# Kernel tuning notes

Measured on AMD Instinct MI355X. Metric: run time of the kernel, lower is better.

## Reference

```python
import jax, jax.numpy as jnp
import numpy as np
import math

B, S, D = 2048, 128, 64          # batch, seq_length, input_dim
H1, H2, OUT = 128, 128, 1        # sa_hidden, ta_hidden, output_dim


def _uniform(key, shape, stdv):
    return jax.random.uniform(key, shape, jnp.float32, -stdv, stdv)


def setup_inputs() -> dict:
    key = jax.random.key(0)
    ks = jax.random.split(key, 20)
    s1 = 1.0 / math.sqrt(H1)
    s2 = 1.0 / math.sqrt(H2)
    inp = {
        "X": jax.random.normal(ks[0], (B, S, D), jnp.float32),
        # SpatialLSTM params (stdv = 1/sqrt(sa_hidden))
        "sa_W": _uniform(ks[1], (D, 4 * H1), s1),
        "sa_U": _uniform(ks[2], (H1, 4 * H1), s1),
        "sa_b": _uniform(ks[3], (4 * H1,), s1),
        "sa_Wa": _uniform(ks[4], (D, D), s1),
        "sa_Ua": _uniform(ks[5], (2 * H1, D), s1),
        "sa_ba": _uniform(ks[6], (D,), s1),
        "sa_Va": _uniform(ks[7], (D, D), s1),
        # TemporalLSTM params (stdv = 1/sqrt(ta_hidden))
        "ta_Wa": _uniform(ks[8], (H1, S), s2),
        "ta_Ua": _uniform(ks[9], (H2, S), s2),
        "ta_ba": _uniform(ks[10], (S,), s2),
        "ta_Va": _uniform(ks[11], (S, S), s2),
        "ta_W": _uniform(ks[12], (H1, 4 * H2), s2),
        "ta_U": _uniform(ks[13], (H2, 4 * H2), s2),
        "ta_b": _uniform(ks[14], (4 * H2,), s2),
        "ta_Wy": _uniform(ks[15], (OUT, 4 * H2), s2),
        "fc_w": _uniform(ks[16], (OUT, H2), s2),
        "fc_b": _uniform(ks[17], (OUT,), s2),
    }
    return inp


def _sta_forward(X, sa_W, sa_U, sa_b, sa_Wa, sa_Ua, sa_ba, sa_Va,
                 ta_Wa, ta_Ua, ta_ba, ta_Va, ta_W, ta_U, ta_b, ta_Wy,
                 fc_w, fc_b):
    x = X[:, :, :D]                       # [B,S,D]
    y0 = X[:, 0, D - 1:].reshape(-1, OUT)  # y[:,0,:] -> [B,OUT]
    batch = x.shape[0]

    # ---- SpatialLSTM: scan over time ----
    def sa_step(carry, x_t):
        h, c = carry
        a = jnp.tanh(x_t @ sa_Wa + jnp.concatenate([h, c], axis=1) @ sa_Ua + sa_ba) @ sa_Va
        alpha = jax.nn.softmax(a, axis=1)            # [B,D]
        xw = alpha * x_t
        gates = xw @ sa_W + h @ sa_U + sa_b          # [B,4H1]
        i = jax.nn.sigmoid(gates[:, :H1])
        f = jax.nn.sigmoid(gates[:, H1:2 * H1])
        g = jnp.tanh(gates[:, 2 * H1:3 * H1])
        o = jax.nn.sigmoid(gates[:, 3 * H1:])
        c = f * c + i * g
        h = o * jnp.tanh(c)
        return (h, c), (h, alpha)

    h0 = jnp.zeros((batch, H1), X.dtype)
    c0 = jnp.zeros((batch, H1), X.dtype)
    _, (hs, alphas) = jax.lax.scan(sa_step, (h0, c0), jnp.swapaxes(x, 0, 1))
    H = jnp.swapaxes(hs, 0, 1)  # [B,S,H1]

    # ---- TemporalLSTM: scan over time, attending over the full H ----
    # note: s_t in the original stays zero for all t, so its s_t @ Ua term is 0.
    def ta_step(carry, h_t):
        lh, lc, y_prev = carry
        beta = jax.nn.softmax(jnp.tanh(h_t @ ta_Wa + ta_ba) @ ta_Va, axis=1)  # [B,S]
        h_att = jnp.einsum('bs,bsd->bd', beta, H)     # weighted sum over time
        gates = h_att @ ta_W + lh @ ta_U + y_prev @ ta_Wy + ta_b
        i = jax.nn.sigmoid(gates[:, :H2])
        f = jax.nn.sigmoid(gates[:, H2:2 * H2])
        g = jnp.tanh(gates[:, 2 * H2:3 * H2])
        o = jax.nn.sigmoid(gates[:, 3 * H2:])
        lc = f * lc + i * g
        lh = o * jnp.tanh(lc)
        y = lh @ fc_w.T + fc_b
        return (lh, lc, y), beta

    lh0 = jnp.zeros((batch, H2), X.dtype)
    lc0 = jnp.zeros((batch, H2), X.dtype)
    (_, _, y_pred), betas = jax.lax.scan(ta_step, (lh0, lc0, y0), jnp.swapaxes(H, 0, 1))
    return y_pred, alphas, betas  # alphas: [S,B,D], betas: [S,B,S]


def reference(X, sa_W, sa_U, sa_b, sa_Wa, sa_Ua, sa_ba, sa_Va,
              ta_Wa, ta_Ua, ta_ba, ta_Va, ta_W, ta_U, ta_b, ta_Wy,
              fc_w, fc_b):
    return _sta_forward(X, sa_W, sa_U, sa_b, sa_Wa, sa_Ua, sa_ba, sa_Va,
                        ta_Wa, ta_Ua, ta_ba, ta_Va, ta_W, ta_U, ta_b, ta_Wy,
                        fc_w, fc_b)
```

## Files before the change

### kernel.cpp

```cpp
#include <hip/hip_runtime.h>


#define BB 2048
#define SS 128
#define DD 64
#define HH 128
#define NG 512
#define M  8
#define NT 512

#define A_OFF    ((size_t)BB)
#define BETA_OFF ((size_t)BB + (size_t)SS*BB*DD)
#define H_BYTES  ((size_t)BB*SS*HH*4)
#define G0_BYTES ((size_t)BB*SS*NG*4)

#define B1G_ELEMS (192*512)
#define B1A_ELEMS (320*64)
#define BVA_ELEMS (64*64)
#define B3_ELEMS  (256*512)
#define BW_ELEMS  (128*128)
#define GH_OFF 0
#define GL_OFF (B1G_ELEMS)
#define AH_OFF (2*B1G_ELEMS)
#define AL_OFF (2*B1G_ELEMS + B1A_ELEMS)
// ... 45 lines not shown
{
  int id = blockIdx.x*256 + threadIdx.x;
  if (id < B1G_ELEMS){
    int k = id >> 9, n = id & 511;
    float v = (k < 128) ? saU[(size_t)k*NG + n] : saW[(size_t)(k-128)*NG + n];
    int kk = k >> 5, kw = k & 31, nt = n >> 4, nc = n & 15;
    int lane = ((kw >> 3) << 4) | nc, j = kw & 7;
    size_t off = ((size_t)(nt*6 + kk)*64 + lane)*8 + j;
    unsigned short hi = bf16rne(v);
    F[GH_OFF + off] = hi; F[GL_OFF + off] = bf16rne(v - bfval(hi));
  }
  if (id < B1A_ELEMS){
    int k = id >> 6, n = id & 63;
    float v = (k < 256) ? saUa[(size_t)k*DD + n] : saWa[(size_t)(k-256)*DD + n];
    int kt = k >> 5, kw = k & 31, nt = n >> 4, nc = n & 15;
    int lane = ((kw >> 3) << 4) | nc, j = kw & 7;
    size_t off = ((size_t)(nt*10 + kt)*64 + lane)*8 + j;
    unsigned short hi = bf16rne(v);
    F[AH_OFF + off] = hi; F[AL_OFF + off] = bf16rne(v - bfval(hi));
  }
  if (id < BVA_ELEMS){
    int k = id >> 6, n = id & 63;
    float v = saVa[(size_t)k*DD + n];
    int kt = k >> 5, kw = k & 31, nt = n >> 4, nc = n & 15;
    int lane = ((kw >> 3) << 4) | nc, j = kw & 7;
    size_t off = ((size_t)(nt*2 + kt)*64 + lane)*8 + j;
    unsigned short hi = bf16rne(v);
    F[VH_OFF + off] = hi; F[VL_OFF + off] = bf16rne(v - bfval(hi));
  }
  if (id < B3_ELEMS){
    int k = id >> 9, n = id & 511;
    float v = (k < HH) ? taU[(size_t)k*NG + n] : taW[(size_t)(k-HH)*NG + n];
    int kt = k >> 5, kw = k & 31, nt = n >> 4, nc = n & 15;
    int lane = ((kw >> 3) << 4) | nc, j = kw & 7;
    size_t off = ((size_t)(nt*8 + kt)*64 + lane)*8 + j;
    unsigned short hi = bf16rne(v);
    F[B3H_OFF + off] = hi; F[B3L_OFF + off] = bf16rne(v - bfval(hi));
  }
  if (id < BW_ELEMS){
    int k = id >> 7, n = id & 127;
    int kt = k >> 5, kw = k & 31, nt = n >> 4, nc = n & 15;
    int lane = ((kw >> 3) << 4) | nc, j = kw & 7;
    size_t off = ((size_t)(nt*4 + kt)*64 + lane)*8 + j;
    F[RW_OFF + off] = bf16rne(taWa[(size_t)k*SS + n]);
    F[RV_OFF + off] = bf16rne(taVa[(size_t)k*SS + n]);
  }
}

struct P1 {
  uint4 afh[12*64];
  uint4 afl[12*64];
  uint4 aah[2*64];
  uint4 aal[2*64];
  float xx[M][DD];
  float cc[M][HH];
  float red[2][M][64];
  float g[M][NG];
  float sbias[NG];
};
struct P2S { float A[32][HH]; float tmp[32][SS]; float bp[32][SS]; };
union __align__(16) SMA { P1 p1; float pad[21504]; };

__global__ __launch_bounds__(NT, 2) __attribute__((amdgpu_waves_per_eu(2, 2)))
void mf_ph1_kernel(
    const float* __restrict__ X,   const float* __restrict__ sab,
    const float* __restrict__ saba,
    const unsigned short* __restrict__ Fr,
    float* __restrict__ out, float* __restrict__ Hws)
{
  __shared__ SMA sm;
  const int tid = threadIdx.x;
  const int b0  = blockIdx.x * M;
  const int w   = tid >> 6, l = tid & 63;

  {
    uint4 z4 = make_uint4(0,0,0,0);
    for (int i = tid; i < 12*64; i += NT){ sm.p1.afh[i] = z4; sm.p1.afl[i] = z4; }
    if (tid < 2*64){ sm.p1.aah[tid] = z4; sm.p1.aal[tid] = z4; }
    for (int i = tid; i < M*HH; i += NT) ((float*)sm.p1.cc)[i] = 0.f;
    sm.p1.sbias[tid] = sab[tid];
  }
  __syncthreads();
  if (tid < 128){
    int r = tid >> 4, d0 = (tid & 15)*4;
    float4 v = *(const float4*)(X + (size_t)(b0+r)*SS*DD + d0);
    *(float4*)&sm.p1.xx[r][d0] = v;
    unsigned short* AFH = (unsigned short*)sm.p1.afh;
    unsigned short* AFL = (unsigned short*)sm.p1.afl;
    int kt = 8 + (d0 >> 5), lane = (((d0 & 31) >> 3) << 4) | r, jj0 = d0 & 7;
    float vv[4] = {v.x, v.y, v.z, v.w};
#pragma unroll
    for (int p = 0; p < 4; ++p){
      unsigned short h_ = bf16rne(vv[p]);
      AFH[(kt*64 + lane)*8 + jj0 + p] = h_;
      AFL[(kt*64 + lane)*8 + jj0 + p] = bf16rne(vv[p] - bfval(h_));
    }
  }
  __syncthreads();

  for (int t = 0; t < SS; ++t){
    f32x4 accg[4];
    {
      f32x4 zf = {0.f,0.f,0.f,0.f};
#pragma unroll
      for (int n4 = 0; n4 < 4; ++n4) accg[n4] = zf;
    }
    {
      const int nt = w & 3, kh = w >> 2;
      f32x4 a0 = {0.f,0.f,0.f,0.f}, a1 = {0.f,0.f,0.f,0.f};
      const uint4* BAH = (const uint4*)(Fr + AH_OFF);
      const uint4* BAL = (const uint4*)(Fr + AL_OFF);
#pragma unroll
      for (int q = 0; q < 5; ++q){
        const int kt = kh*5 + q;
        bf16x8 ah = as_bf(sm.p1.afh[kt*64 + l]);
        bf16x8 av = as_bf(sm.p1.afl[kt*64 + l]);
        bf16x8 bh = as_bf(BAH[(nt*10 + kt)*64 + l]);
        bf16x8 bl = as_bf(BAL[(nt*10 + kt)*64 + l]);
        if (q & 1){
          a1 = __builtin_amdgcn_mfma_f32_16x16x32_bf16(ah, bh, a1, 0, 0, 0);
          a1 = __builtin_amdgcn_mfma_f32_16x16x32_bf16(av, bh, a1, 0, 0, 0);
          a1 = __builtin_amdgcn_mfma_f32_16x16x32_bf16(ah, bl, a1, 0, 0, 0);
        } else {
          a0 = __builtin_amdgcn_mfma_f32_16x16x32_bf16(ah, bh, a0, 0, 0, 0);
          a0 = __builtin_amdgcn_mfma_f32_16x16x32_bf16(av, bh, a0, 0, 0, 0);
          a0 = __builtin_amdgcn_mfma_f32_16x16x32_bf16(ah, bl, a0, 0, 0, 0);
        }
      }
      f32x4 acc = a0 + a1;
      const int row0 = (l >> 4)*4, c0 = l & 15;
      if (row0 < 8){
#pragma unroll
        for (int jj = 0; jj < 4; ++jj)
          sm.p1.red[kh][row0+jj][nt*16 + c0] = acc[jj];
      }
      const uint4* GH = (const uint4*)(Fr + GH_OFF);
      const uint4* GL = (const uint4*)(Fr + GL_OFF);
#pragma unroll
      for (int kk = 0; kk < 4; ++kk){
        bf16x8 ah = as_bf(sm.p1.afh[kk*64 + l]);
        bf16x8 av = as_bf(sm.p1.afl[kk*64 + l]);
#pragma unroll
        for (int n4 = 0; n4 < 4; ++n4){
          const int ntg = w*4 + n4;
          bf16x8 bh = as_bf(GH[(ntg*6 + kk)*64 + l]);
          bf16x8 bl = as_bf(GL[(ntg*6 + kk)*64 + l]);
          accg[n4] = __builtin_amdgcn_mfma_f32_16x16x32_bf16(ah, bh, accg[n4], 0, 0, 0);
          accg[n4] = __builtin_amdgcn_mfma_f32_16x16x32_bf16(av, bh, accg[n4], 0, 0, 0);
          accg[n4] = __builtin_amdgcn_mfma_f32_16x16x32_bf16(ah, bl, accg[n4], 0, 0, 0);
        }
      }
    }
    __syncthreads();

    {
      const int r = w, col = l;
      float s = sm.p1.red[0][r][col] + sm.p1.red[1][r][col] + saba[col];
      float av = tanhx(s);
      unsigned short h_ = bf16rne(av);
      int kt = col >> 5, lane = (((col & 31) >> 3) << 4) | r, jj = col & 7;
      ((unsigned short*)sm.p1.aah)[(kt*64 + lane)*8 + jj] = h_;
      ((unsigned short*)sm.p1.aal)[(kt*64 + lane)*8 + jj] = bf16rne(av - bfval(h_));
    }
    __syncthreads();

    {
      const int nt = w & 3, kt = w >> 2;
      f32x4 acc = {0.f,0.f,0.f,0.f};
      bf16x8 ah = as_bf(sm.p1.aah[kt*64 + l]);
      bf16x8 av = as_bf(sm.p1.aal[kt*64 + l]);
      bf16x8 bh = as_bf(((const uint4*)(Fr + VH_OFF))[(nt*2 + kt)*64 + l]);
      bf16x8 bl = as_bf(((const uint4*)(Fr + VL_OFF))[(nt*2 + kt)*64 + l]);
      acc = __builtin_amdgcn_mfma_f32_16x16x32_bf16(ah, bh, acc, 0, 0, 0);
      acc = __builtin_amdgcn_mfma_f32_16x16x32_bf16(av, bh, acc, 0, 0, 0);
      acc = __builtin_amdgcn_mfma_f32_16x16x32_bf16(ah, bl, acc, 0, 0, 0);
      const int row0 = (l >> 4)*4, c0 = l & 15;
      if (row0 < 8){
#pragma unroll
        for (int jj = 0; jj < 4; ++jj)
          sm.p1.red[kt][row0+jj][nt*16 + c0] = acc[jj];
      }
    }
    __syncthreads();

    {
      const int r = w, col = l;
      float s = sm.p1.red[0][r][col] + sm.p1.red[1][r][col];
      float mm = wmax64(s);
      float e  = __expf(s - mm);
      float alv = e * (1.0f / wsum64(e));
      out[A_OFF + (size_t)t*BB*DD + (size_t)(b0+r)*DD + col] = alv;
      float xwv = alv * sm.p1.xx[r][col];
      unsigned short h_ = bf16rne(xwv);
      int kt = 10 + (col >> 5), lane = (((col & 31) >> 3) << 4) | r, jj = col & 7;
      ((unsigned short*)sm.p1.afh)[(kt*64 + lane)*8 + jj] = h_;
      ((unsigned short*)sm.p1.afl)[(kt*64 + lane)*8 + jj] = bf16rne(xwv - bfval(h_));
    }
    __syncthreads();

    float4 pf;
    const bool dox = (tid < 128) && (t + 1 < SS);
    if (dox){
      int r = tid >> 4, d0 = (tid & 15)*4;
      pf = *(const float4*)(X + (size_t)(b0+r)*SS*DD + (size_t)(t+1)*DD + d0);
    }
    {
      const uint4* GH = (const uint4*)(Fr + GH_OFF);
      const uint4* GL = (const uint4*)(Fr + GL_OFF);
#pragma unroll
      for (int kk = 4; kk < 6; ++kk){
        const int afi = kk + 6;
        bf16x8 ah = as_bf(sm.p1.afh[afi*64 + l]);
        bf16x8 av = as_bf(sm.p1.afl[afi*64 + l]);
#pragma unroll
        for (int n4 = 0; n4 < 4; ++n4){
          const int ntg = w*4 + n4;
          bf16x8 bh = as_bf(GH[(ntg*6 + kk)*64 + l]);
          bf16x8 bl = as_bf(GL[(ntg*6 + kk)*64 + l]);
          accg[n4] = __builtin_amdgcn_mfma_f32_16x16x32_bf16(ah, bh, accg[n4], 0, 0, 0);
          accg[n4] = __builtin_amdgcn_mfma_f32_16x16x32_bf16(av, bh, accg[n4], 0, 0, 0);
          accg[n4] = __builtin_amdgcn_mfma_f32_16x16x32_bf16(ah, bl, accg[n4], 0, 0, 0);
        }
      }
      const int row0 = (l >> 4)*4, c0 = l & 15;
      if (row0 < 8){
#pragma unroll
        for (int n4 = 0; n4 < 4; ++n4){
          int col = w*64 + n4*16 + c0;
          float b = sm.p1.sbias[col];
#pragma unroll
          for (int jj = 0; jj < 4; ++jj)
            sm.p1.g[row0+jj][col] = accg[n4][jj] + b;
        }
      }
    }
    __syncthreads();

    {
      unsigned short* AFH = (unsigned short*)sm.p1.afh;
      unsigned short* AFL = (unsigned short*)sm.p1.afl;
#pragma unroll
      for (int h2 = 0; h2 < 2; ++h2){
        int idx = h2*NT + tid;
        int r = idx >> 7, j = idx & 127;
        float iv = sigf (sm.p1.g[r][j]);
        float fv = sigf (sm.p1.g[r][j + 128]);
        float gv = tanhx(sm.p1.g[r][j + 256]);
        float ov = sigf (sm.p1.g[r][j + 384]);
        float cn = fv * sm.p1.cc[r][j] + iv * gv;
        float hn = ov * tanhx(cn);
        sm.p1.cc[r][j] = cn;
        Hws[(size_t)(b0+r)*SS*HH + (size_t)t*HH + j] = hn;
        int lane = (((j & 31) >> 3) << 4) | r, jj = j & 7;
        int ktH = j >> 5, ktC = 4 + (j >> 5);
        unsigned short hh_ = bf16rne(hn);
        unsigned short ch_ = bf16rne(cn);
        AFH[(ktH*64 + lane)*8 + jj] = hh_;
        AFL[(ktH*64 + lane)*8 + jj] = bf16rne(hn - bfval(hh_));
        AFH[(ktC*64 + lane)*8 + jj] = ch_;
        AFL[(ktC*64 + lane)*8 + jj] = bf16rne(cn - bfval(ch_));
      }
      if (dox){
        int r = tid >> 4, d0 = (tid & 15)*4;
        *(float4*)&sm.p1.xx[r][d0] = pf;
        int kt = 8 + (d0 >> 5), lane = (((d0 & 31) >> 3) << 4) | r, jj0 = d0 & 7;
        float vv[4] = {pf.x, pf.y, pf.z, pf.w};
#pragma unroll
        for (int p = 0; p < 4; ++p){
          unsigned short h_ = bf16rne(vv[p]);
          AFH[(kt*64 + lane)*8 + jj0 + p] = h_;
          AFL[(kt*64 + lane)*8 + jj0 + p] = bf16rne(vv[p] - bfval(h_));
        }
      }
    }
    __syncthreads();
  }
}

struct PH2SM {
  union {
    struct { uint4 fA[8][4][64]; uint4 fB[8][4][64]; } f;
    float HO[128][132];
  } u;
  unsigned short S[128][136];
  float bias[SS];
};

__global__ __launch_bounds__(NT, 2) void ph2_kernel(
    const float* __restrict__ taba, const unsigned short* __restrict__ Fr,
    float* __restrict__ out, float* __restrict__ Hws)
{
  __shared__ PH2SM sm;
  const int tid = threadIdx.x;
  const int b   = blockIdx.x;
  const int w   = tid >> 6, l = tid & 63;
  const int g   = l >> 4, c0 = l & 15;
  float* Hb = Hws + (size_t)b * SS * HH;

  if (tid < SS) sm.bias[tid] = taba[tid];
  {
    const float4* src = (const float4*)Hb;
#pragma unroll
    for (int i = 0; i < 8; ++i){
      int fidx = i*NT + tid;
      float4 v = src[fidx];
      int e0 = fidx*4, row = e0 >> 7, col = e0 & 127;
      sm.S[row][col+0] = bf16rne(v.x);
      sm.S[row][col+1] = bf16rne(v.y);
      sm.S[row][col+2] = bf16rne(v.z);
      sm.S[row][col+3] = bf16rne(v.w);
    }
  }
  __syncthreads();

#pragma unroll
  for (int i = 0; i < 4; ++i){
    int slot = i*NT + tid;
    int mt = slot >> 8, kt = (slot >> 6) & 3, ll = slot & 63;
    int row = mt*16 + (ll & 15), k0 = kt*32 + (ll >> 4)*8;
    ((uint4*)sm.u.f.fA)[slot] = *(const uint4*)&sm.S[row][k0];
  }
#pragma unroll
  for (int i = 0; i < 4; ++i){
    int slot = i*NT + tid;
    int nt = slot >> 8, kt = (slot >> 6) & 3, ll = slot & 63;
    int col = nt*16 + (ll & 15), s0 = kt*32 + (ll >> 4)*8;
// ... 63 lines not shown
    for (int nt = 1; nt < 8; ++nt) m = fmaxf(m, acc[nt][j]);
#pragma unroll
    for (int ms = 1; ms < 16; ms <<= 1) m = fmaxf(m, __shfl_xor(m, ms, 64));
    float e[8], s = 0.f;
#pragma unroll
    for (int nt = 0; nt < 8; ++nt){ e[nt] = __expf(acc[nt][j] - m); s += e[nt]; }
#pragma unroll
    for (int ms = 1; ms < 16; ms <<= 1) s += __shfl_xor(s, ms, 64);
    float inv = 1.0f / s;
    int row = w*16 + g*4 + j;
    size_t bo = BETA_OFF + (size_t)row*BB*SS + (size_t)b*SS;
#pragma unroll
    for (int nt = 0; nt < 8; ++nt){
      float bv = e[nt] * inv;
      out[bo + nt*16 + c0] = bv;
      sm.S[row][nt*16 + c0] = bf16rne(bv);
    }
  }
  __syncthreads();

#pragma unroll
  for (int i = 0; i < 4; ++i){
    int slot = i*NT + tid;
    int mt = slot >> 8, kt = (slot >> 6) & 3, ll = slot & 63;
    int row = mt*16 + (ll & 15), k0 = kt*32 + (ll >> 4)*8;
    ((uint4*)sm.u.f.fA)[slot] = *(const uint4*)&sm.S[row][k0];
  }
  __syncthreads();

#pragma unroll
  for (int nt = 0; nt < 8; ++nt) acc[nt] = zero4;
#pragma unroll
  for (int kt = 0; kt < 4; ++kt){
    bf16x8 a = as_bf(sm.u.f.fA[w][kt][l]);
#pragma unroll
    for (int nt = 0; nt < 8; ++nt){
      bf16x8 bv = as_bf(sm.u.f.fB[nt][kt][l]);
      acc[nt] = __builtin_amdgcn_mfma_f32_16x16x32_bf16(a, bv, acc[nt], 0, 0, 0);
    }
  }
  __syncthreads();

#pragma unroll
  for (int nt = 0; nt < 8; ++nt)
#pragma unroll
    for (int j = 0; j < 4; ++j)
      sm.u.HO[w*16 + g*4 + j][nt*16 + c0] = acc[nt][j];
  __syncthreads();
#pragma unroll
  for (int it = 0; it < 8; ++it){
    int flat = it*NT + tid;
    int row = flat >> 5, cq = flat & 31;
    *(float4*)(Hb + (size_t)row*HH + cq*4) = *(const float4*)&sm.u.HO[row][cq*4];
  }
}

struct GMM { uint4 afh[8][4][64]; uint4 afl[8][4][64]; float SG[128][132]; };

__global__ __launch_bounds__(NT, 2) void g0mm_kernel(
    const float* __restrict__ Ha, const unsigned short* __restrict__ Fr,
    const float* __restrict__ tab, float* __restrict__ G0)
{
  __shared__ GMM sm;
  const int tid = threadIdx.x;
  const size_t r0 = (size_t)blockIdx.x * 128;
  const int w = tid >> 6, l = tid & 63;
  const int row0 = (l >> 4)*4, c0 = l & 15;

  {
    const float4* src = (const float4*)(Ha + r0*HH);
    unsigned short* AFH = (unsigned short*)sm.afh;
    unsigned short* AFL = (unsigned short*)sm.afl;
#pragma unroll
    for (int i = 0; i < 8; ++i){
      int f = i*NT + tid;
      float4 v = src[f];
      int e0 = f*4, rl = e0 >> 7, k0 = e0 & 127;
      int mt = rl >> 4, kt = k0 >> 5;
      int lane = (((k0 & 31) >> 3) << 4) | (rl & 15), j0 = k0 & 7;
      size_t base = ((size_t)(mt*4 + kt)*64 + lane)*8 + j0;
      float vv[4] = {v.x, v.y, v.z, v.w};
#pragma unroll
      for (int p = 0; p < 4; ++p){
        unsigned short h_ = bf16rne(vv[p]);
        AFH[base + p] = h_;
        AFL[base + p] = bf16rne(vv[p] - bfval(h_));
      }
    }
  }
  __syncthreads();

  const uint4* BH = (const uint4*)(Fr + B3H_OFF);
  const uint4* BL = (const uint4*)(Fr + B3L_OFF);
#pragma unroll
  for (int p = 0; p < 4; ++p){
    const int nt = p*8 + w;
    uint4 bh[4], bl[4];
#pragma unroll
    for (int kt = 0; kt < 4; ++kt){
      bh[kt] = BH[(nt*8 + 4 + kt)*64 + l];
      bl[kt] = BL[(nt*8 + 4 + kt)*64 + l];
    }
    const float tb = tab[nt*16 + c0];
    f32x4 zero4 = {0.f,0.f,0.f,0.f};
    f32x4 acc[8];
#pragma unroll
    for (int mt = 0; mt < 8; ++mt) acc[mt] = zero4;
#pragma unroll
    for (int mt = 0; mt < 8; ++mt){
#pragma unroll
      for (int kt = 0; kt < 4; ++kt){
        bf16x8 ah = as_bf(sm.afh[mt][kt][l]);
        bf16x8 av = as_bf(sm.afl[mt][kt][l]);
        bf16x8 vbh = as_bf(bh[kt]);
        bf16x8 vbl = as_bf(bl[kt]);
        acc[mt] = __builtin_amdgcn_mfma_f32_16x16x32_bf16(ah, vbh, acc[mt], 0, 0, 0);
        acc[mt] = __builtin_amdgcn_mfma_f32_16x16x32_bf16(av, vbh, acc[mt], 0, 0, 0);
        acc[mt] = __builtin_amdgcn_mfma_f32_16x16x32_bf16(ah, vbl, acc[mt], 0, 0, 0);
      }
    }
#pragma unroll
    for (int mt = 0; mt < 8; ++mt)
#pragma unroll
      for (int j = 0; j < 4; ++j)
        sm.SG[mt*16 + row0 + j][w*16 + c0] = acc[mt][j] + tb;
    __syncthreads();
#pragma unroll
    for (int it = 0; it < 8; ++it){
      int flat = it*NT + tid;
      int row = flat >> 5, cq = flat & 31;
      *(float4*)(G0 + (r0 + row)*NG + p*128 + cq*4) = *(const float4*)&sm.SG[row][cq*4];
    }
    __syncthreads();
  }
}

struct P3H {
  uint4 afh[4*64];
  uint4 afl[4*64];
  float lh[M][HH];
  float lc[M][HH];
  float g[M][NG];
  float wy[NG];
  float fcv[HH];
  float yp[M];
};
union __align__(16) SMCH { P3H s; float pad[21504]; };

__global__ __launch_bounds__(NT, 2) __attribute__((amdgpu_waves_per_eu(2, 2)))
void mf_ph3h_kernel(
    const float* __restrict__ X, const unsigned short* __restrict__ Fr,
    const float* __restrict__ G0,
    const float* __restrict__ taWy,
    const float* __restrict__ fcw, const float* __restrict__ fcb,
    float* __restrict__ out)
{
  __shared__ SMCH sm;
  const int tid = threadIdx.x;
  const int b0  = blockIdx.x * M;
  const int w   = tid >> 6, l = tid & 63;
  const int row0 = (l >> 4)*4, c0 = l & 15;

  {
    uint4 z4 = make_uint4(0,0,0,0);
    if (tid < 4*64){ sm.s.afh[tid] = z4; sm.s.afl[tid] = z4; }
    for (int i = tid; i < M*HH; i += NT){
      ((float*)sm.s.lh)[i] = 0.f; ((float*)sm.s.lc)[i] = 0.f;
    }
    sm.s.wy[tid] = taWy[tid];
    if (tid < HH) sm.s.fcv[tid] = fcw[tid];
    if (tid < M)  sm.s.yp[tid] = X[(size_t)(b0+tid)*SS*DD + (DD-1)];
  }
  __syncthreads();

  for (int t = 0; t < SS; ++t){
    {
      float g0v[16];
      if (row0 < 8){
#pragma unroll
        for (int n4 = 0; n4 < 4; ++n4){
#pragma unroll
          for (int j = 0; j < 4; ++j)
            g0v[n4*4+j] = G0[((size_t)(b0+row0+j)*SS + t)*NG + (w*64 + n4*16 + c0)];
        }
      }
      f32x4 zero4 = {0.f,0.f,0.f,0.f};
      f32x4 acc[4];
#pragma unroll
      for (int n4 = 0; n4 < 4; ++n4) acc[n4] = zero4;
      const uint4* BH = (const uint4*)(Fr + B3H_OFF);
      const uint4* BL = (const uint4*)(Fr + B3L_OFF);
#pragma unroll
      for (int kt = 0; kt < 4; ++kt){
        bf16x8 ah = as_bf(sm.s.afh[kt*64 + l]);
        bf16x8 av = as_bf(sm.s.afl[kt*64 + l]);
#pragma unroll
        for (int n4 = 0; n4 < 4; ++n4){
          const int ntg = w*4 + n4;
          bf16x8 bh = as_bf(BH[(ntg*8 + kt)*64 + l]);
          bf16x8 bl = as_bf(BL[(ntg*8 + kt)*64 + l]);
          acc[n4] = __builtin_amdgcn_mfma_f32_16x16x32_bf16(ah, bh, acc[n4], 0, 0, 0);
          acc[n4] = __builtin_amdgcn_mfma_f32_16x16x32_bf16(av, bh, acc[n4], 0, 0, 0);
          acc[n4] = __builtin_amdgcn_mfma_f32_16x16x32_bf16(ah, bl, acc[n4], 0, 0, 0);
        }
      }
      if (row0 < 8){
#pragma unroll
        for (int n4 = 0; n4 < 4; ++n4){
          int col = w*64 + n4*16 + c0;
          float wv = sm.s.wy[col];
#pragma unroll
          for (int j = 0; j < 4; ++j)
            sm.s.g[row0+j][col] = acc[n4][j] + g0v[n4*4+j] + sm.s.yp[row0+j]*wv;
        }
      }
    }
    __syncthreads();

    {
      unsigned short* AFH = (unsigned short*)sm.s.afh;
      unsigned short* AFL = (unsigned short*)sm.s.afl;
#pragma unroll
      for (int h2 = 0; h2 < 2; ++h2){
        int idx = h2*NT + tid;
        int r = idx >> 7, j = idx & 127;
        float iv = sigf (sm.s.g[r][j]);
        float fv = sigf (sm.s.g[r][j + 128]);
        float gv = tanhx(sm.s.g[r][j + 256]);
        float ov = sigf (sm.s.g[r][j + 384]);
        float cn = fv * sm.s.lc[r][j] + iv * gv;
        float hn = ov * tanhx(cn);
        sm.s.lc[r][j] = cn; sm.s.lh[r][j] = hn;
        int kt = j >> 5, lane = (((j & 31) >> 3) << 4) | r, jj = j & 7;
        unsigned short h_ = bf16rne(hn);
        AFH[(kt*64 + lane)*8 + jj] = h_;
        AFL[(kt*64 + lane)*8 + jj] = bf16rne(hn - bfval(h_));
      }
    }
    __syncthreads();

    {
      const int r = w, lx = l;
      float p = sm.s.lh[r][lx]*sm.s.fcv[lx] + sm.s.lh[r][lx+64]*sm.s.fcv[lx+64];
      p = wsum64(p);
      if (lx == 0) sm.s.yp[r] = p + fcb[0];
    }
    __syncthreads();
  }

  if (tid < M) out[b0 + tid] = sm.s.yp[tid];
}

struct P3 {
  uint4 afh[8*64];
  uint4 afl[8*64];
  float lh[M][HH];
  float lc[M][HH];
  float g[M][NG];
  float sb[NG];
  float wy[NG];
  float fcv[HH];
  float yp[M];
};
union __align__(16) SMC { P3 s; float pad[21504]; };

__global__ __launch_bounds__(NT, 2) void mf_ph3_kernel(
    const float* __restrict__ X, const float* __restrict__ Ha,
    const unsigned short* __restrict__ Fr,
    const float* __restrict__ tab, const float* __restrict__ taWy,
    const float* __restrict__ fcw, const float* __restrict__ fcb,
    float* __restrict__ out)
{
  __shared__ SMC sm;
  const int tid = threadIdx.x;
  const int b0  = blockIdx.x * M;
  const int w   = tid >> 6, l = tid & 63;

  {
    uint4 z4 = make_uint4(0,0,0,0);
    sm.s.afh[tid] = z4; sm.s.afl[tid] = z4;
    for (int i = tid; i < M*HH; i += NT){
      ((float*)sm.s.lh)[i] = 0.f; ((float*)sm.s.lc)[i] = 0.f;
    }
    sm.s.sb[tid] = tab[tid];
    sm.s.wy[tid] = taWy[tid];
    if (tid < HH) sm.s.fcv[tid] = fcw[tid];
    if (tid < M)  sm.s.yp[tid] = X[(size_t)(b0+tid)*SS*DD + (DD-1)];
  }
  __syncthreads();
  if (tid < 256){
    int r = tid >> 5, d0 = (tid & 31)*4;
    float4 v = *(const float4*)(Ha + (size_t)(b0+r)*SS*HH + d0);
    unsigned short* AFH = (unsigned short*)sm.s.afh;
    unsigned short* AFL = (unsigned short*)sm.s.afl;
    int kt = 4 + (d0 >> 5), lane = (((d0 & 31) >> 3) << 4) | r, jj0 = d0 & 7;
    float vv[4] = {v.x, v.y, v.z, v.w};
#pragma unroll
    for (int p = 0; p < 4; ++p){
// ... 399 lines not shown
      float gv = tanhx(s.g[r][j + 2*HH]);
      float ov = sigf (s.g[r][j + 3*HH]);
      float cn = fv * s.lc[r][j] + iv * gv;
      float hn = ov * tanhx(cn);
      s.lc[r][j] = cn; s.lh[r][j] = hn;
    }
    if (t + 1 < SS && tid < M*HH/4){
      int r = tid >> 5, q = tid & 31;
      ((float4*)s.ha)[tid] =
        *(const float4*)(Ha + (size_t)(b0+r)*SS*HH + (size_t)(t+1)*HH + q*4);
    }
    __syncthreads();
    {
      const int r = tid >> 6, lx = tid & 63;
      float p = s.lh[r][lx]*fcw[lx] + s.lh[r][lx+64]*fcw[lx+64];
      p = wsum64(p);
      if (lx == 0) s.yp[r] = p + fcb[0];
    }
    __syncthreads();
  }
  if (tid < M) out[b0 + tid] = s.yp[tid];
}

extern "C" void kernel_launch(void* const* d_in, const int* in_sizes, int n_in,
                              void* d_out, int out_size, void* d_ws, size_t ws_size,
                              hipStream_t stream) {
  (void)in_sizes; (void)n_in; (void)out_size;
  const float* X    = (const float*)d_in[0];
  const float* saW  = (const float*)d_in[1];
  const float* saU  = (const float*)d_in[2];
  const float* sab  = (const float*)d_in[3];
  const float* saWa = (const float*)d_in[4];
  const float* saUa = (const float*)d_in[5];
  const float* saba = (const float*)d_in[6];
  const float* saVa = (const float*)d_in[7];
  const float* taWa = (const float*)d_in[8];
  const float* taba = (const float*)d_in[10];
  const float* taVa = (const float*)d_in[11];
  const float* taW  = (const float*)d_in[12];
  const float* taU  = (const float*)d_in[13];
  const float* tab  = (const float*)d_in[14];
  const float* taWy = (const float*)d_in[15];
  const float* fcw  = (const float*)d_in[16];
  const float* fcb  = (const float*)d_in[17];
  float* out = (float*)d_out;

  if (ws_size >= NEED2_BYTES){
    unsigned short* Fr = (unsigned short*)d_ws;
    float* Hws = (float*)((char*)d_ws + FRAG_BYTES);
    hipLaunchKernelGGL(repack_kernel, dim3(512), dim3(256), 0, stream,
                       saW, saU, saWa, saUa, saVa, taU, taW, taWa, taVa, Fr);
    hipLaunchKernelGGL(mf_ph1_kernel, dim3(BB / M), dim3(NT), 0, stream,
                       X, sab, saba, Fr, out, Hws);
    hipLaunchKernelGGL(ph2_kernel, dim3(BB), dim3(NT), 0, stream,
                       taba, Fr, out, Hws);
    if (ws_size >= NEED3_BYTES){
      float* G0 = (float*)((char*)d_ws + FRAG_BYTES + H_BYTES);
      hipLaunchKernelGGL(g0mm_kernel, dim3((BB*SS)/128), dim3(NT), 0, stream,
                         Hws, Fr, tab, G0);
      hipLaunchKernelGGL(mf_ph3h_kernel, dim3(BB / M), dim3(NT), 0, stream,
                         X, Fr, G0, taWy, fcw, fcb, out);
    } else {
      hipLaunchKernelGGL(mf_ph3_kernel, dim3(BB / M), dim3(NT), 0, stream,
                         X, Hws, Fr, tab, taWy, fcw, fcb, out);
    }
  } else {
    float* Hws = (float*)d_ws;
    hipLaunchKernelGGL(fb_ph12_kernel, dim3(BB / M), dim3(NT), 0, stream,
                       X, saW, saU, sab, saWa, saUa, saba, saVa,
                       taWa, taba, taVa, out, Hws);
    hipLaunchKernelGGL(fb_ph3_kernel, dim3(BB / M), dim3(NT), 0, stream,
                       X, Hws, taW, taU, tab, taWy, fcw, fcb, out);
  }
}
```

Before: 1.621 ms.

## Fuse temporal attention with G0 projection, cache spatial weights in LDS, prefetch G0

Adds a ph2g kernel that computes the temporal attention (beta and h_att) per batch element and immediately multiplies h_att by the input weights to write the precomputed gate term G0. This replaces the separate ph2 and g0mm kernels and avoids writing h_att to global memory and reading it back. The spatial-phase kernel now stages the attention weight fragments (Ua/Wa and Va) in shared memory once instead of re-reading them from global memory every timestep. The temporal recurrent kernel prefetches the next step's G0 values into registers. The extra LDS in the spatial kernel may reduce occupancy.

Measured after the change: 1.432 ms. 1.13x faster.

```diff
diff --git a/kernel.cpp b/kernel.cpp
--- a/kernel.cpp
+++ b/kernel.cpp
@@ -121,6 +121,10 @@
   uint4 afl[12*64];
   uint4 aah[2*64];
   uint4 aal[2*64];
+  uint4 awh[2560];
+  uint4 awl[2560];
+  uint4 vh[512];
+  uint4 vl[512];
   float xx[M][DD];
   float cc[M][HH];
   float red[2][M][64];
@@ -128,7 +132,6 @@
   float sbias[NG];
 };
 struct P2S { float A[32][HH]; float tmp[32][SS]; float bp[32][SS]; };
-union __align__(16) SMA { P1 p1; float pad[21504]; };
 
 __global__ __launch_bounds__(NT, 2) __attribute__((amdgpu_waves_per_eu(2, 2)))
 void mf_ph1_kernel(
@@ -137,25 +140,30 @@
     const unsigned short* __restrict__ Fr,
     float* __restrict__ out, float* __restrict__ Hws)
 {
-  __shared__ SMA sm;
+  __shared__ P1 sm;
   const int tid = threadIdx.x;
   const int b0  = blockIdx.x * M;
   const int w   = tid >> 6, l = tid & 63;
 
   {
     uint4 z4 = make_uint4(0,0,0,0);
-    for (int i = tid; i < 12*64; i += NT){ sm.p1.afh[i] = z4; sm.p1.afl[i] = z4; }
-    if (tid < 2*64){ sm.p1.aah[tid] = z4; sm.p1.aal[tid] = z4; }
-    for (int i = tid; i < M*HH; i += NT) ((float*)sm.p1.cc)[i] = 0.f;
-    sm.p1.sbias[tid] = sab[tid];
+    for (int i = tid; i < 12*64; i += NT){ sm.afh[i] = z4; sm.afl[i] = z4; }
+    if (tid < 2*64){ sm.aah[tid] = z4; sm.aal[tid] = z4; }
+    for (int i = tid; i < M*HH; i += NT) ((float*)sm.cc)[i] = 0.f;
+    sm.sbias[tid] = sab[tid];
+    const uint4* sh = (const uint4*)(Fr + AH_OFF);
+    const uint4* sl = (const uint4*)(Fr + AL_OFF);
+    for (int i = tid; i < 2560; i += NT){ sm.awh[i] = sh[i]; sm.awl[i] = sl[i]; }
+    sm.vh[tid] = ((const uint4*)(Fr + VH_OFF))[tid];
+    sm.vl[tid] = ((const uint4*)(Fr + VL_OFF))[tid];
   }
   __syncthreads();
   if (tid < 128){
     int r = tid >> 4, d0 = (tid & 15)*4;
     float4 v = *(const float4*)(X + (size_t)(b0+r)*SS*DD + d0);
-    *(float4*)&sm.p1.xx[r][d0] = v;
-    unsigned short* AFH = (unsigned short*)sm.p1.afh;
-    unsigned short* AFL = (unsigned short*)sm.p1.afl;
+    *(float4*)&sm.xx[r][d0] = v;
+    unsigned short* AFH = (unsigned short*)sm.afh;
+    unsigned short* AFL = (unsigned short*)sm.afl;
     int kt = 8 + (d0 >> 5), lane = (((d0 & 31) >> 3) << 4) | r, jj0 = d0 & 7;
     float vv[4] = {v.x, v.y, v.z, v.w};
 #pragma unroll
@@ -177,15 +185,13 @@
     {
       const int nt = w & 3, kh = w >> 2;
       f32x4 a0 = {0.f,0.f,0.f,0.f}, a1 = {0.f,0.f,0.f,0.f};
-      const uint4* BAH = (const uint4*)(Fr + AH_OFF);
-      const uint4* BAL = (const uint4*)(Fr + AL_OFF);
 #pragma unroll
       for (int q = 0; q < 5; ++q){
         const int kt = kh*5 + q;
-        bf16x8 ah = as_bf(sm.p1.afh[kt*64 + l]);
-        bf16x8 av = as_bf(sm.p1.afl[kt*64 + l]);
-        bf16x8 bh = as_bf(BAH[(nt*10 + kt)*64 + l]);
-        bf16x8 bl = as_bf(BAL[(nt*10 + kt)*64 + l]);
+        bf16x8 ah = as_bf(sm.afh[kt*64 + l]);
+        bf16x8 av = as_bf(sm.afl[kt*64 + l]);
+        bf16x8 bh = as_bf(sm.awh[(nt*10 + kt)*64 + l]);
+        bf16x8 bl = as_bf(sm.awl[(nt*10 + kt)*64 + l]);
         if (q & 1){
           a1 = __builtin_amdgcn_mfma_f32_16x16x32_bf16(ah, bh, a1, 0, 0, 0);
           a1 = __builtin_amdgcn_mfma_f32_16x16x32_bf16(av, bh, a1, 0, 0, 0);
@@ -201,14 +207,14 @@
       if (row0 < 8){
 #pragma unroll
         for (int jj = 0; jj < 4; ++jj)
-          sm.p1.red[kh][row0+jj][nt*16 + c0] = acc[jj];
+          sm.red[kh][row0+jj][nt*16 + c0] = acc[jj];
       }
       const uint4* GH = (const uint4*)(Fr + GH_OFF);
       const uint4* GL = (const uint4*)(Fr + GL_OFF);
 #pragma unroll
       for (int kk = 0; kk < 4; ++kk){
-        bf16x8 ah = as_bf(sm.p1.afh[kk*64 + l]);
-        bf16x8 av = as_bf(sm.p1.afl[kk*64 + l]);
+        bf16x8 ah = as_bf(sm.afh[kk*64 + l]);
+        bf16x8 av = as_bf(sm.afl[kk*64 + l]);
 #pragma unroll
         for (int n4 = 0; n4 < 4; ++n4){
           const int ntg = w*4 + n4;
@@ -224,22 +230,22 @@
 
     {
       const int r = w, col = l;
-      float s = sm.p1.red[0][r][col] + sm.p1.red[1][r][col] + saba[col];
+      float s = sm.red[0][r][col] + sm.red[1][r][col] + saba[col];
       float av = tanhx(s);
       unsigned short h_ = bf16rne(av);
       int kt = col >> 5, lane = (((col & 31) >> 3) << 4) | r, jj = col & 7;
-      ((unsigned short*)sm.p1.aah)[(kt*64 + lane)*8 + jj] = h_;
-      ((unsigned short*)sm.p1.aal)[(kt*64 + lane)*8 + jj] = bf16rne(av - bfval(h_));
+      ((unsigned short*)sm.aah)[(kt*64 + lane)*8 + jj] = h_;
+      ((unsigned short*)sm.aal)[(kt*64 + lane)*8 + jj] = bf16rne(av - bfval(h_));
     }
     __syncthreads();
 
     {
       const int nt = w & 3, kt = w >> 2;
       f32x4 acc = {0.f,0.f,0.f,0.f};
-      bf16x8 ah = as_bf(sm.p1.aah[kt*64 + l]);
-      bf16x8 av = as_bf(sm.p1.aal[kt*64 + l]);
-      bf16x8 bh = as_bf(((const uint4*)(Fr + VH_OFF))[(nt*2 + kt)*64 + l]);
-      bf16x8 bl = as_bf(((const uint4*)(Fr + VL_OFF))[(nt*2 + kt)*64 + l]);
+      bf16x8 ah = as_bf(sm.aah[kt*64 + l]);
+      bf16x8 av = as_bf(sm.aal[kt*64 + l]);
+      bf16x8 bh = as_bf(sm.vh[(nt*2 + kt)*64 + l]);
+      bf16x8 bl = as_bf(sm.vl[(nt*2 + kt)*64 + l]);
       acc = __builtin_amdgcn_mfma_f32_16x16x32_bf16(ah, bh, acc, 0, 0, 0);
       acc = __builtin_amdgcn_mfma_f32_16x16x32_bf16(av, bh, acc, 0, 0, 0);
       acc = __builtin_amdgcn_mfma_f32_16x16x32_bf16(ah, bl, acc, 0, 0, 0);
@@ -247,23 +253,23 @@
       if (row0 < 8){
 #pragma unroll
         for (int jj = 0; jj < 4; ++jj)
-          sm.p1.red[kt][row0+jj][nt*16 + c0] = acc[jj];
+          sm.red[kt][row0+jj][nt*16 + c0] = acc[jj];
       }
     }
     __syncthreads();
 
     {
       const int r = w, col = l;
-      float s = sm.p1.red[0][r][col] + sm.p1.red[1][r][col];
+      float s = sm.red[0][r][col] + sm.red[1][r][col];
       float mm = wmax64(s);
       float e  = __expf(s - mm);
       float alv = e * (1.0f / wsum64(e));
       out[A_OFF + (size_t)t*BB*DD + (size_t)(b0+r)*DD + col] = alv;
-      float xwv = alv * sm.p1.xx[r][col];
+      float xwv = alv * sm.xx[r][col];
       unsigned short h_ = bf16rne(xwv);
       int kt = 10 + (col >> 5), lane = (((col & 31) >> 3) << 4) | r, jj = col & 7;
-      ((unsigned short*)sm.p1.afh)[(kt*64 + lane)*8 + jj] = h_;
-      ((unsigned short*)sm.p1.afl)[(kt*64 + lane)*8 + jj] = bf16rne(xwv - bfval(h_));
+      ((unsigned short*)sm.afh)[(kt*64 + lane)*8 + jj] = h_;
+      ((unsigned short*)sm.afl)[(kt*64 + lane)*8 + jj] = bf16rne(xwv - bfval(h_));
     }
     __syncthreads();
 
@@ -279,8 +285,8 @@
 #pragma unroll
       for (int kk = 4; kk < 6; ++kk){
         const int afi = kk + 6;
-        bf16x8 ah = as_bf(sm.p1.afh[afi*64 + l]);
-        bf16x8 av = as_bf(sm.p1.afl[afi*64 + l]);
+        bf16x8 ah = as_bf(sm.afh[afi*64 + l]);
+        bf16x8 av = as_bf(sm.afl[afi*64 + l]);
 #pragma unroll
         for (int n4 = 0; n4 < 4; ++n4){
           const int ntg = w*4 + n4;
@@ -296,29 +302,29 @@
 #pragma unroll
         for (int n4 = 0; n4 < 4; ++n4){
           int col = w*64 + n4*16 + c0;
-          float b = sm.p1.sbias[col];
+          float b = sm.sbias[col];
 #pragma unroll
           for (int jj = 0; jj < 4; ++jj)
-            sm.p1.g[row0+jj][col] = accg[n4][jj] + b;
-        }
-      }
-    }
-    __syncthreads();
-
-    {
-      unsigned short* AFH = (unsigned short*)sm.p1.afh;
-      unsigned short* AFL = (unsigned short*)sm.p1.afl;
+            sm.g[row0+jj][col] = accg[n4][jj] + b;
+        }
+      }
+    }
+    __syncthreads();
+
+    {
+      unsigned short* AFH = (unsigned short*)sm.afh;
+      unsigned short* AFL = (unsigned short*)sm.afl;
 #pragma unroll
       for (int h2 = 0; h2 < 2; ++h2){
         int idx = h2*NT + tid;
         int r = idx >> 7, j = idx & 127;
-        float iv = sigf (sm.p1.g[r][j]);
-        float fv = sigf (sm.p1.g[r][j + 128]);
-        float gv = tanhx(sm.p1.g[r][j + 256]);
-        float ov = sigf (sm.p1.g[r][j + 384]);
-        float cn = fv * sm.p1.cc[r][j] + iv * gv;
+        float iv = sigf (sm.g[r][j]);
+        float fv = sigf (sm.g[r][j + 128]);
+        float gv = tanhx(sm.g[r][j + 256]);
+        float ov = sigf (sm.g[r][j + 384]);
+        float cn = fv * sm.cc[r][j] + iv * gv;
         float hn = ov * tanhx(cn);
-        sm.p1.cc[r][j] = cn;
+        sm.cc[r][j] = cn;
         Hws[(size_t)(b0+r)*SS*HH + (size_t)t*HH + j] = hn;
         int lane = (((j & 31) >> 3) << 4) | r, jj = j & 7;
         int ktH = j >> 5, ktC = 4 + (j >> 5);
@@ -331,7 +337,7 @@
       }
       if (dox){
         int r = tid >> 4, d0 = (tid & 15)*4;
-        *(float4*)&sm.p1.xx[r][d0] = pf;
+        *(float4*)&sm.xx[r][d0] = pf;
         int kt = 8 + (d0 >> 5), lane = (((d0 & 31) >> 3) << 4) | r, jj0 = d0 & 7;
         float vv[4] = {pf.x, pf.y, pf.z, pf.w};
 #pragma unroll
@@ -341,6 +347,220 @@
           AFL[(kt*64 + lane)*8 + jj0 + p] = bf16rne(vv[p] - bfval(h_));
         }
       }
+    }
+    __syncthreads();
+  }
+}
+
+struct PH2G {
+  union { unsigned short S[128][136]; float SG[128][68]; } u1;
+  unsigned short S2[128][136];
+  uint4 fA[8][4][64];
+  uint4 fB[8][4][64];
+  float bias[SS];
+};
+
+__global__ __launch_bounds__(NT, 2) void ph2g_kernel(
+    const float* __restrict__ taba, const unsigned short* __restrict__ Fr,
+    const float* __restrict__ tab,
+    float* __restrict__ out, float* __restrict__ Hws, float* __restrict__ G0)
+{
+  __shared__ PH2G sm;
+  const int tid = threadIdx.x;
+  const int b   = blockIdx.x;
+  const int w   = tid >> 6, l = tid & 63;
+  const int g   = l >> 4, c0 = l & 15;
+  const float* Hb = Hws + (size_t)b * SS * HH;
+
+  if (tid < SS) sm.bias[tid] = taba[tid];
+  {
+    const float4* src = (const float4*)Hb;
+#pragma unroll
+    for (int i = 0; i < 8; ++i){
+      int fidx = i*NT + tid;
+      float4 v = src[fidx];
+      int e0 = fidx*4, row = e0 >> 7, col = e0 & 127;
+      sm.u1.S[row][col+0] = bf16rne(v.x);
+      sm.u1.S[row][col+1] = bf16rne(v.y);
+      sm.u1.S[row][col+2] = bf16rne(v.z);
+      sm.u1.S[row][col+3] = bf16rne(v.w);
+    }
+  }
+  __syncthreads();
+
+#pragma unroll
+  for (int i = 0; i < 4; ++i){
+    int slot = i*NT + tid;
+    int mt = slot >> 8, kt = (slot >> 6) & 3, ll = slot & 63;
+    int row = mt*16 + (ll & 15), k0 = kt*32 + (ll >> 4)*8;
+    ((uint4*)sm.fA)[slot] = *(const uint4*)&sm.u1.S[row][k0];
+  }
+#pragma unroll
+  for (int i = 0; i < 4; ++i){
+    int slot = i*NT + tid;
+    int nt = slot >> 8, kt = (slot >> 6) & 3, ll = slot & 63;
+    int col = nt*16 + (ll & 15), s0 = kt*32 + (ll >> 4)*8;
+    unsigned u[4];
+#pragma unroll
+    for (int p = 0; p < 4; ++p)
+      u[p] = (unsigned)sm.u1.S[s0+2*p][col] | ((unsigned)sm.u1.S[s0+2*p+1][col] << 16);
+    ((uint4*)sm.fB)[slot] = make_uint4(u[0], u[1], u[2], u[3]);
+  }
+  __syncthreads();
+
+  f32x4 acc[8];
+  f32x4 zero4 = {0.f, 0.f, 0.f, 0.f};
+
+#pragma unroll
+  for (int nt = 0; nt < 8; ++nt) acc[nt] = zero4;
+  {
+    const uint4* BW = (const uint4*)(Fr + RW_OFF);
+#pragma unroll
+    for (int kt = 0; kt < 4; ++kt){
+      bf16x8 a = as_bf(sm.fA[w][kt][l]);
+#pragma unroll
+      for (int nt = 0; nt < 8; ++nt){
+        bf16x8 bv = as_bf(BW[(nt*4 + kt)*64 + l]);
+        acc[nt] = __builtin_amdgcn_mfma_f32_16x16x32_bf16(a, bv, acc[nt], 0, 0, 0);
+      }
+    }
+  }
+#pragma unroll
+  for (int nt = 0; nt < 8; ++nt){
+    int col = nt*16 + c0;
+    float bv = sm.bias[col];
+#pragma unroll
+    for (int j = 0; j < 4; ++j)
+      sm.u1.S[w*16 + g*4 + j][col] = bf16rne(tanhx(acc[nt][j] + bv));
+  }
+  __syncthreads();
+
+#pragma unroll
+  for (int i = 0; i < 4; ++i){
+    int slot = i*NT + tid;
+    int mt = slot >> 8, kt = (slot >> 6) & 3, ll = slot & 63;
+    int row = mt*16 + (ll & 15), k0 = kt*32 + (ll >> 4)*8;
+    ((uint4*)sm.fA)[slot] = *(const uint4*)&sm.u1.S[row][k0];
+  }
+  __syncthreads();
+
+#pragma unroll
+  for (int nt = 0; nt < 8; ++nt) acc[nt] = zero4;
+  {
+    const uint4* BV = (const uint4*)(Fr + RV_OFF);
+#pragma unroll
+    for (int kt = 0; kt < 4; ++kt){
+      bf16x8 a = as_bf(sm.fA[w][kt][l]);
+#pragma unroll
+      for (int nt = 0; nt < 8; ++nt){
+        bf16x8 bv = as_bf(BV[(nt*4 + kt)*64 + l]);
+        acc[nt] = __builtin_amdgcn_mfma_f32_16x16x32_bf16(a, bv, acc[nt], 0, 0, 0);
+      }
+    }
+  }
+
+#pragma unroll
+  for (int j = 0; j < 4; ++j){
+    float m = acc[0][j];
+#pragma unroll
+    for (int nt = 1; nt < 8; ++nt) m = fmaxf(m, acc[nt][j]);
+#pragma unroll
+    for (int ms = 1; ms < 16; ms <<= 1) m = fmaxf(m, __shfl_xor(m, ms, 64));
+    float e[8], s = 0.f;
+#pragma unroll
+    for (int nt = 0; nt < 8; ++nt){ e[nt] = __expf(acc[nt][j] - m); s += e[nt]; }
+#pragma unroll
+    for (int ms = 1; ms < 16; ms <<= 1) s += __shfl_xor(s, ms, 64);
+    float inv = 1.0f / s;
+    int row = w*16 + g*4 + j;
+    size_t bo = BETA_OFF + (size_t)row*BB*SS + (size_t)b*SS;
+#pragma unroll
+    for (int nt = 0; nt < 8; ++nt){
+      float bv = e[nt] * inv;
+      out[bo + nt*16 + c0] = bv;
+      sm.u1.S[row][nt*16 + c0] = bf16rne(bv);
+    }
+  }
+  __syncthreads();
+
+#pragma unroll
+  for (int i = 0; i < 4; ++i){
+    int slot = i*NT + tid;
+    int mt = slot >> 8, kt = (slot >> 6) & 3, ll = slot & 63;
+    int row = mt*16 + (ll & 15), k0 = kt*32 + (ll >> 4)*8;
+    ((uint4*)sm.fA)[slot] = *(const uint4*)&sm.u1.S[row][k0];
+  }
+  __syncthreads();
+
+#pragma unroll
+  for (int nt = 0; nt < 8; ++nt) acc[nt] = zero4;
+#pragma unroll
+  for (int kt = 0; kt < 4; ++kt){
+    bf16x8 a = as_bf(sm.fA[w][kt][l]);
+#pragma unroll
+    for (int nt = 0; nt < 8; ++nt){
+      bf16x8 bv = as_bf(sm.fB[nt][kt][l]);
+      acc[nt] = __builtin_amdgcn_mfma_f32_16x16x32_bf16(a, bv, acc[nt], 0, 0, 0);
+    }
+  }
+#pragma unroll
+  for (int nt = 0; nt < 8; ++nt){
+#pragma unroll
+    for (int j = 0; j < 4; ++j){
+      int row = w*16 + g*4 + j, col = nt*16 + c0;
+      float v = acc[nt][j];
+      unsigned short h_ = bf16rne(v);
+      sm.u1.S[row][col] = h_;
+      sm.S2[row][col]   = bf16rne(v - bfval(h_));
+    }
+  }
+  __syncthreads();
+
+#pragma unroll
+  for (int i = 0; i < 4; ++i){
+    int slot = i*NT + tid;
+    int mt = slot >> 8, kt = (slot >> 6) & 3, ll = slot & 63;
+    int row = mt*16 + (ll & 15), k0 = kt*32 + (ll >> 4)*8;
+    ((uint4*)sm.fA)[slot] = *(const uint4*)&sm.u1.S[row][k0];
+    ((uint4*)sm.fB)[slot] = *(const uint4*)&sm.S2[row][k0];
+  }
+  __syncthreads();
+
+  const uint4* BH = (const uint4*)(Fr + B3H_OFF);
+  const uint4* BL = (const uint4*)(Fr + B3L_OFF);
+  const size_t r0 = (size_t)b * SS;
+#pragma unroll
+  for (int p = 0; p < 8; ++p){
+    f32x4 acc2[4];
+#pragma unroll
+    for (int q = 0; q < 4; ++q) acc2[q] = zero4;
+#pragma unroll
+    for (int q = 0; q < 4; ++q){
+      const int ntg = p*4 + q;
+#pragma unroll
+      for (int kt = 0; kt < 4; ++kt){
+        bf16x8 ah = as_bf(sm.fA[w][kt][l]);
+        bf16x8 av = as_bf(sm.fB[w][kt][l]);
+        bf16x8 bh = as_bf(BH[(ntg*8 + 4 + kt)*64 + l]);
+        bf16x8 bl = as_bf(BL[(ntg*8 + 4 + kt)*64 + l]);
+        acc2[q] = __builtin_amdgcn_mfma_f32_16x16x32_bf16(ah, bh, acc2[q], 0, 0, 0);
+        acc2[q] = __builtin_amdgcn_mfma_f32_16x16x32_bf16(av, bh, acc2[q], 0, 0, 0);
+        acc2[q] = __builtin_amdgcn_mfma_f32_16x16x32_bf16(ah, bl, acc2[q], 0, 0, 0);
+      }
+    }
+#pragma unroll
+    for (int q = 0; q < 4; ++q){
+      float tb = tab[p*64 + q*16 + c0];
+#pragma unroll
+      for (int j = 0; j < 4; ++j)
+        sm.u1.SG[w*16 + g*4 + j][q*16 + c0] = acc2[q][j] + tb;
+    }
+    __syncthreads();
+#pragma unroll
+    for (int it = 0; it < 4; ++it){
+      int flat = it*NT + tid;
+      int row = flat >> 4, cq = flat & 15;
+      *(float4*)(G0 + (r0 + row)*NG + p*64 + cq*4) = *(const float4*)&sm.u1.SG[row][cq*4];
     }
     __syncthreads();
   }
@@ -510,86 +730,6 @@
     int flat = it*NT + tid;
     int row = flat >> 5, cq = flat & 31;
     *(float4*)(Hb + (size_t)row*HH + cq*4) = *(const float4*)&sm.u.HO[row][cq*4];
-  }
-}
-
-struct GMM { uint4 afh[8][4][64]; uint4 afl[8][4][64]; float SG[128][132]; };
-
-__global__ __launch_bounds__(NT, 2) void g0mm_kernel(
-    const float* __restrict__ Ha, const unsigned short* __restrict__ Fr,
-    const float* __restrict__ tab, float* __restrict__ G0)
-{
-  __shared__ GMM sm;
-  const int tid = threadIdx.x;
-  const size_t r0 = (size_t)blockIdx.x * 128;
-  const int w = tid >> 6, l = tid & 63;
-  const int row0 = (l >> 4)*4, c0 = l & 15;
-
-  {
-    const float4* src = (const float4*)(Ha + r0*HH);
-    unsigned short* AFH = (unsigned short*)sm.afh;
-    unsigned short* AFL = (unsigned short*)sm.afl;
-#pragma unroll
-    for (int i = 0; i < 8; ++i){
-      int f = i*NT + tid;
-      float4 v = src[f];
-      int e0 = f*4, rl = e0 >> 7, k0 = e0 & 127;
-      int mt = rl >> 4, kt = k0 >> 5;
-      int lane = (((k0 & 31) >> 3) << 4) | (rl & 15), j0 = k0 & 7;
-      size_t base = ((size_t)(mt*4 + kt)*64 + lane)*8 + j0;
-      float vv[4] = {v.x, v.y, v.z, v.w};
-#pragma unroll
-      for (int p = 0; p < 4; ++p){
-        unsigned short h_ = bf16rne(vv[p]);
-        AFH[base + p] = h_;
-        AFL[base + p] = bf16rne(vv[p] - bfval(h_));
-      }
-    }
-  }
-  __syncthreads();
-
-  const uint4* BH = (const uint4*)(Fr + B3H_OFF);
-  const uint4* BL = (const uint4*)(Fr + B3L_OFF);
-#pragma unroll
-  for (int p = 0; p < 4; ++p){
-    const int nt = p*8 + w;
-    uint4 bh[4], bl[4];
-#pragma unroll
-    for (int kt = 0; kt < 4; ++kt){
-      bh[kt] = BH[(nt*8 + 4 + kt)*64 + l];
-      bl[kt] = BL[(nt*8 + 4 + kt)*64 + l];
-    }
-    const float tb = tab[nt*16 + c0];
-    f32x4 zero4 = {0.f,0.f,0.f,0.f};
-    f32x4 acc[8];
-#pragma unroll
-    for (int mt = 0; mt < 8; ++mt) acc[mt] = zero4;
-#pragma unroll
-    for (int mt = 0; mt < 8; ++mt){
-#pragma unroll
-      for (int kt = 0; kt < 4; ++kt){
-        bf16x8 ah = as_bf(sm.afh[mt][kt][l]);
-        bf16x8 av = as_bf(sm.afl[mt][kt][l]);
-        bf16x8 vbh = as_bf(bh[kt]);
-        bf16x8 vbl = as_bf(bl[kt]);
-        acc[mt] = __builtin_amdgcn_mfma_f32_16x16x32_bf16(ah, vbh, acc[mt], 0, 0, 0);
-        acc[mt] = __builtin_amdgcn_mfma_f32_16x16x32_bf16(av, vbh, acc[mt], 0, 0, 0);
-        acc[mt] = __builtin_amdgcn_mfma_f32_16x16x32_bf16(ah, vbl, acc[mt], 0, 0, 0);
-      }
-    }
-#pragma unroll
-    for (int mt = 0; mt < 8; ++mt)
-#pragma unroll
-      for (int j = 0; j < 4; ++j)
-        sm.SG[mt*16 + row0 + j][w*16 + c0] = acc[mt][j] + tb;
-    __syncthreads();
-#pragma unroll
-    for (int it = 0; it < 8; ++it){
-      int flat = it*NT + tid;
-      int row = flat >> 5, cq = flat & 31;
-      *(float4*)(G0 + (r0 + row)*NG + p*128 + cq*4) = *(const float4*)&sm.SG[row][cq*4];
-    }
-    __syncthreads();
   }
 }
 
@@ -629,19 +769,18 @@
     if (tid < HH) sm.s.fcv[tid] = fcw[tid];
     if (tid < M)  sm.s.yp[tid] = X[(size_t)(b0+tid)*SS*DD + (DD-1)];
   }
+  float g0v[16];
+  if (row0 < 8){
+#pragma unroll
+    for (int n4 = 0; n4 < 4; ++n4)
+#pragma unroll
+      for (int j = 0; j < 4; ++j)
+        g0v[n4*4+j] = G0[((size_t)(b0+row0+j)*SS + 0)*NG + (w*64 + n4*16 + c0)];
+  }
   __syncthreads();
 
   for (int t = 0; t < SS; ++t){
     {
-      float g0v[16];
-      if (row0 < 8){
-#pragma unroll
-        for (int n4 = 0; n4 < 4; ++n4){
-#pragma unroll
-          for (int j = 0; j < 4; ++j)
-            g0v[n4*4+j] = G0[((size_t)(b0+row0+j)*SS + t)*NG + (w*64 + n4*16 + c0)];
-        }
-      }
       f32x4 zero4 = {0.f,0.f,0.f,0.f};
       f32x4 acc[4];
 #pragma unroll
@@ -675,6 +814,15 @@
     }
     __syncthreads();
 
+    float g0n[16];
+    const bool dog = (t + 1 < SS) && (row0 < 8);
+    if (dog){
+#pragma unroll
+      for (int n4 = 0; n4 < 4; ++n4)
+#pragma unroll
+        for (int j = 0; j < 4; ++j)
+          g0n[n4*4+j] = G0[((size_t)(b0+row0+j)*SS + (t+1))*NG + (w*64 + n4*16 + c0)];
+    }
     {
       unsigned short* AFH = (unsigned short*)sm.s.afh;
       unsigned short* AFL = (unsigned short*)sm.s.afl;
@@ -702,6 +850,10 @@
       float p = sm.s.lh[r][lx]*sm.s.fcv[lx] + sm.s.lh[r][lx+64]*sm.s.fcv[lx+64];
       p = wsum64(p);
       if (lx == 0) sm.s.yp[r] = p + fcb[0];
+    }
+    if (dog){
+#pragma unroll
+      for (int q = 0; q < 16; ++q) g0v[q] = g0n[q];
     }
     __syncthreads();
   }
@@ -1207,15 +1359,15 @@
                        saW, saU, saWa, saUa, saVa, taU, taW, taWa, taVa, Fr);
     hipLaunchKernelGGL(mf_ph1_kernel, dim3(BB / M), dim3(NT), 0, stream,
                        X, sab, saba, Fr, out, Hws);
-    hipLaunchKernelGGL(ph2_kernel, dim3(BB), dim3(NT), 0, stream,
-                       taba, Fr, out, Hws);
     if (ws_size >= NEED3_BYTES){
       float* G0 = (float*)((char*)d_ws + FRAG_BYTES + H_BYTES);
-      hipLaunchKernelGGL(g0mm_kernel, dim3((BB*SS)/128), dim3(NT), 0, stream,
-                         Hws, Fr, tab, G0);
+      hipLaunchKernelGGL(ph2g_kernel, dim3(BB), dim3(NT), 0, stream,
+                         taba, Fr, tab, out, Hws, G0);
       hipLaunchKernelGGL(mf_ph3h_kernel, dim3(BB / M), dim3(NT), 0, stream,
                          X, Fr, G0, taWy, fcw, fcb, out);
     } else {
+      hipLaunchKernelGGL(ph2_kernel, dim3(BB), dim3(NT), 0, stream,
+                         taba, Fr, out, Hws);
       hipLaunchKernelGGL(mf_ph3_kernel, dim3(BB / M), dim3(NT), 0, stream,
                          X, Hws, Fr, tab, taWy, fcw, fcb, out);
     }
```
